# Kernel tuning notes

Measured on AMD Instinct MI355X. Metric: run time of the kernel, lower is better.

## Reference

```python
import jax, jax.numpy as jnp
import numpy as np

N, IN_DIM, OUT_DIM = 8192, 128, 64
ALPHA = 0.2  # LeakyReLU negative slope
NEG_INF = -1e12


def setup_inputs() -> dict:
    key = jax.random.key(0)
    k1, k2, k3, k4 = jax.random.split(key, 4)
    x = jax.random.normal(k1, (N, IN_DIM), dtype=jnp.float32)
    adj = jax.random.randint(k2, (N, N), 0, 2, dtype=jnp.int32)
    W = jax.random.normal(k3, (IN_DIM, OUT_DIM), dtype=jnp.float32) * 0.1
    a = jax.random.normal(k4, (2 * OUT_DIM, 1), dtype=jnp.float32) * 0.1
    return {"x": x, "adj": adj, "W": W, "a": a}


def reference(x, adj, W, a):
    Wh = x @ W                                   # [N, out_dim]
    Wh1 = Wh @ a[:OUT_DIM, :]                    # [N, 1] source scores
    Wh2 = Wh @ a[OUT_DIM:, :]                    # [N, 1] target scores
    e = Wh1 + Wh2.T                              # [N, N] additive attention
    e = jnp.where(e > 0, e, ALPHA * e)           # LeakyReLU
    scores = jnp.where(adj > 0, e, NEG_INF)      # mask non-edges
    attention = jax.nn.softmax(scores, axis=1)   # row-wise softmax
    h_prime = attention @ Wh                     # [N, out_dim]
    return jax.nn.elu(h_prime)
```

## Files before the change

kernel.cpp:

```cpp
#include <hip/hip_runtime.h>


#define N 8192
#define IN_DIM 128
#define OUT_DIM 64
#define ALPHA 0.2f
#define LOG2E 1.44269504088896f
#define JC 4
#define LDP 264

typedef _Float16 half8 __attribute__((ext_vector_type(8)));
typedef _Float16 h2 __attribute__((ext_vector_type(2)));
typedef float f32x4 __attribute__((ext_vector_type(4)));

static __device__ __forceinline__ h2 bc_h2(unsigned u) {
  return __builtin_bit_cast(h2, u);
}

__global__ __launch_bounds__(64) void wh_kernel(
    const float* __restrict__ x, const float* __restrict__ W,
    const float* __restrict__ a, _Float16* __restrict__ Wh_t,
    float* __restrict__ s1L, float* __restrict__ s2L) {
  __shared__ float xs[IN_DIM];
  const int i = blockIdx.x;
  const int t = threadIdx.x;

  xs[t]      = x[(size_t)i * IN_DIM + t];
  xs[t + 64] = x[(size_t)i * IN_DIM + 64 + t];
  __syncthreads();

  float wh = 0.f;
#pragma unroll
  for (int d = 0; d < IN_DIM; ++d) wh = fmaf(xs[d], W[d * OUT_DIM + t], wh);

  Wh_t[(size_t)t * N + i] = (_Float16)wh;

  float p1 = wh * a[t];
  float p2 = wh * a[64 + t];
#pragma unroll
  for (int off = 32; off; off >>= 1) {
    p1 += __shfl_down(p1, off);
    p2 += __shfl_down(p2, off);
  }
  if (t == 0) {
    s1L[i] = p1 * LOG2E;
    s2L[i] = p2 * LOG2E;
  }
}

__global__ __launch_bounds__(256) void max_kernel(
    const float* __restrict__ s1L, const float* __restrict__ s2L,
    float* __restrict__ mm) {
  __shared__ float red[8];
  const int t = threadIdx.x;
  float m1 = -1e30f, m2 = -1e30f;
  for (int idx = t; idx < N; idx += 256) {
    m1 = fmaxf(m1, s1L[idx]);
    m2 = fmaxf(m2, s2L[idx]);
  }
#pragma unroll
  for (int off = 32; off; off >>= 1) {
    m1 = fmaxf(m1, __shfl_down(m1, off));
    m2 = fmaxf(m2, __shfl_down(m2, off));
  }
  if ((t & 63) == 0) {
    red[t >> 6] = m1;
    red[4 + (t >> 6)] = m2;
  }
  __syncthreads();
  if (t == 0) {
    m1 = fmaxf(fmaxf(red[0], red[1]), fmaxf(red[2], red[3]));
    m2 = fmaxf(fmaxf(red[4], red[5]), fmaxf(red[6], red[7]));
    float e = m1 + m2;
    mm[0] = m1;
    mm[1] = fmaxf(e, ALPHA * e);
  }
}

__global__ __launch_bounds__(256) void ftab_kernel(
    const float* __restrict__ s1L, const float* __restrict__ s2L,
    const float* __restrict__ mm, unsigned int* __restrict__ Fi,
    _Float16* __restrict__ TTh) {
  const int j = blockIdx.x * 256 + threadIdx.x;
  const float m1 = mm[0], ML = mm[1];

  const float v1 = s1L[j] - m1;
  h2 f;
  f[0] = (_Float16)exp2f(v1);
  f[1] = (_Float16)exp2f(0.2f * v1);
  Fi[j] = __builtin_bit_cast(unsigned int, f);

  TTh[(j >> 2) * 8 + (j & 3)]     = (_Float16)exp2f(s2L[j] - (ML - m1));
  TTh[(j >> 2) * 8 + 4 + (j & 3)] =
      (_Float16)exp2f(0.2f * s2L[j] - (ML - 0.2f * m1));
}

__global__ __launch_bounds__(256) void bpack_kernel(
    const _Float16* __restrict__ Wh_t, _Float16* __restrict__ Bpack) {
  const int kt = blockIdx.x;
  const int t = threadIdx.x;
  const int fg = t >> 6;
  const int lane = t & 63;
  const int q = (t >> 4) & 3;
  const int r16 = t & 15;
  const half8 v =
      *(const half8*)(Wh_t + (size_t)(fg * 16 + r16) * N + kt * 32 + q * 8);
  *(half8*)(Bpack + ((size_t)(kt * 4 + fg) * 64 + lane) * 8) = v;
}

__global__ __launch_bounds__(256, 2) void attn_kernel(
    const int* __restrict__ adj, const _Float16* __restrict__ Bpack,
    const unsigned int* __restrict__ Fi, const uint4* __restrict__ TT,
    float* __restrict__ accp, float* __restrict__ lp) {
  __shared__ __align__(16) _Float16 Ps[4 * 16 * LDP];

  const int t = threadIdx.x;
  const int w = t >> 6;
  const int lane = t & 63;
  const int q = lane >> 4;
  const int r16 = lane & 15;
  const int i0 = blockIdx.x * 64 + w * 16;
  const int c = blockIdx.y;
  const int jb = c * (N / JC);

  _Float16* Pw = Ps + w * 16 * LDP;
  const _Float16* ldA = Pw + r16 * LDP + q * 8;

  half8 bones;
#pragma unroll
  for (int e = 0; e < 8; ++e)
    bones[e] = (r16 == 0) ? (_Float16)1.0f : (_Float16)0.0f;

  const unsigned fi_all = Fi[i0 + r16];
  const int* apb = adj + (size_t)i0 * N + jb + lane * 4;
  const uint4* ttb = TT + (jb >> 2) + lane;

  f32x4 acc[5] = {{0.f, 0.f, 0.f, 0.f}, {0.f, 0.f, 0.f, 0.f},
                  {0.f, 0.f, 0.f, 0.f}, {0.f, 0.f, 0.f, 0.f},
                  {0.f, 0.f, 0.f, 0.f}};

  for (int jt = 0; jt < (N / JC) / 256; ++jt) {
    const uint4 tt = ttb[jt * 64];

#pragma unroll
    for (int b = 0; b < 4; ++b) {
      int4 av[4];
#pragma unroll
      for (int rr = 0; rr < 4; ++rr)
        av[rr] = *(const int4*)(apb + (size_t)(b * 4 + rr) * N + jt * 256);
#pragma unroll
      for (int rr = 0; rr < 4; ++rr) {
        const int row = b * 4 + rr;
        const unsigned u = __shfl(fi_all, row);
        const h2 f1 = bc_h2((u & 0xFFFFu) * 0x00010001u);
        const h2 f2 = bc_h2((u >> 16) * 0x00010001u);
        const unsigned mlo = (unsigned)(av[rr].x | (av[rr].y << 16)) * 0x3C00u;
        const unsigned mhi = (unsigned)(av[rr].z | (av[rr].w << 16)) * 0x3C00u;
        const h2 plo =
            __builtin_elementwise_max(f1 * bc_h2(tt.x), f2 * bc_h2(tt.z)) *
            bc_h2(mlo);
        const h2 phi =
            __builtin_elementwise_max(f1 * bc_h2(tt.y), f2 * bc_h2(tt.w)) *
            bc_h2(mhi);
        uint2 pw;
        pw.x = __builtin_bit_cast(unsigned, plo);
        pw.y = __builtin_bit_cast(unsigned, phi);
        *(uint2*)(Pw + row * LDP + lane * 4) = pw;
      }
    }

    const int ktb = c * 64 + jt * 8;
#pragma unroll
    for (int ks = 0; ks < 8; ++ks) {
      const half8 aF = *(const half8*)(ldA + ks * 32);
      const _Float16* bp = Bpack + ((size_t)((ktb + ks) * 4) * 64 + lane) * 8;
#pragma unroll
      for (int fg = 0; fg < 4; ++fg) {
        const half8 bf = *(const half8*)(bp + (size_t)fg * 512);
        acc[fg] =
            __builtin_amdgcn_mfma_f32_16x16x32_f16(aF, bf, acc[fg], 0, 0, 0);
      }
      acc[4] =
          __builtin_amdgcn_mfma_f32_16x16x32_f16(aF, bones, acc[4], 0, 0, 0);
    }
  }

#pragma unroll
  for (int fg = 0; fg < 4; ++fg) {
#pragma unroll
    for (int r = 0; r < 4; ++r) {
      accp[((size_t)c * N + i0 + q * 4 + r) * OUT_DIM + fg * 16 + r16] =
          acc[fg][r];
    }
  }
  if (r16 == 0) {
#pragma unroll
    for (int r = 0; r < 4; ++r) lp[(size_t)c * N + i0 + q * 4 + r] = acc[4][r];
  }
}

__global__ __launch_bounds__(256) void reduce_kernel(
    const float* __restrict__ accp, const float* __restrict__ lp,
    float* __restrict__ out) {
  const int tid = blockIdx.x * 256 + threadIdx.x;
  const int i = tid >> 6;
  float s = 0.f, l = 0.f;
#pragma unroll
  for (int c = 0; c < JC; ++c) s += accp[(size_t)c * N * OUT_DIM + tid];
#pragma unroll
  for (int c = 0; c < JC; ++c) l += lp[(size_t)c * N + i];
  float v = s / l;
  out[tid] = v > 0.f ? v : expm1f(v);
}

extern "C" void kernel_launch(void* const* d_in, const int* in_sizes, int n_in,
                              void* d_out, int out_size, void* d_ws,
                              size_t ws_size, hipStream_t stream) {
  const float* x = (const float*)d_in[0];
  const int* adj = (const int*)d_in[1];
  const float* W = (const float*)d_in[2];
  const float* a = (const float*)d_in[3];
  float* out = (float*)d_out;

  char* ws = (char*)d_ws;
  _Float16* Wh_t = (_Float16*)ws;
  float* s1L = (float*)(ws + (1u << 20));
  float* s2L = (float*)(ws + (1u << 20) + (64u << 10));
  float* mm = (float*)(ws + (1u << 20) + (128u << 10));
  unsigned* Fi = (unsigned*)(ws + (1u << 20) + (192u << 10));
  _Float16* TTh = (_Float16*)(ws + (1u << 20) + (256u << 10));
  _Float16* Bpack = (_Float16*)(ws + (2u << 20));
  float* accp = (float*)(ws + (4u << 20));
  float* lp = (float*)(ws + (20u << 20));

  wh_kernel<<<N, 64, 0, stream>>>(x, W, a, Wh_t, s1L, s2L);
  max_kernel<<<1, 256, 0, stream>>>(s1L, s2L, mm);
  ftab_kernel<<<N / 256, 256, 0, stream>>>(s1L, s2L, mm, Fi, TTh);
  bpack_kernel<<<N / 32, 256, 0, stream>>>(Wh_t, Bpack);
  attn_kernel<<<dim3(N / 64, JC), 256, 0, stream>>>(
      adj, Bpack, Fi, (const uint4*)TTh, accp, lp);
  reduce_kernel<<<N * OUT_DIM / 256, 256, 0, stream>>>(accp, lp, out);
}
```

Measured before the change: 442.3 us.

## Share attention tile across waves and keep Wh operands in registers

The attention kernel is reorganized so each block covers 128 rows by 512 columns. The four waves jointly build one 16-row probability tile in shared memory, and each wave multiplies it against its own 16-feature slice of Wh, held in registers for the whole block. Adjacency rows for the next 16-row group are prefetched into registers during the MFMA phase, and only one wave computes the row-sum MFMA. This removes the repeated global loads of packed Wh and the per-wave private P tiles. In exchange, the column split grows to 16 chunks, which quadruples partial-sum traffic for the reduce kernel and adds two block barriers per row group.

```diff
diff --git a/kernel.cpp b/kernel.cpp
--- a/kernel.cpp
+++ b/kernel.cpp
@@ -6,8 +6,9 @@
 #define OUT_DIM 64
 #define ALPHA 0.2f
 #define LOG2E 1.44269504088896f
-#define JC 4
-#define LDP 264
+#define JC 16
+#define LDP 520
+#define RG 8
 
 typedef _Float16 half8 __attribute__((ext_vector_type(8)));
 typedef _Float16 h2 __attribute__((ext_vector_type(2)));
@@ -108,94 +109,97 @@
   *(half8*)(Bpack + ((size_t)(kt * 4 + fg) * 64 + lane) * 8) = v;
 }
 
-__global__ __launch_bounds__(256, 2) void attn_kernel(
+__global__ __launch_bounds__(256, 3) void attn_kernel(
     const int* __restrict__ adj, const _Float16* __restrict__ Bpack,
     const unsigned int* __restrict__ Fi, const uint4* __restrict__ TT,
     float* __restrict__ accp, float* __restrict__ lp) {
-  __shared__ __align__(16) _Float16 Ps[4 * 16 * LDP];
+  __shared__ __align__(16) _Float16 Pb[16 * LDP];
 
   const int t = threadIdx.x;
   const int w = t >> 6;
   const int lane = t & 63;
   const int q = lane >> 4;
   const int r16 = lane & 15;
-  const int i0 = blockIdx.x * 64 + w * 16;
+  const int half_ = lane >> 5;
+  const int l32 = lane & 31;
+  const int ib0 = blockIdx.x * 128;
   const int c = blockIdx.y;
-  const int jb = c * (N / JC);
-
-  _Float16* Pw = Ps + w * 16 * LDP;
-  const _Float16* ldA = Pw + r16 * LDP + q * 8;
+  const int jb = c * 512;
+  const int jw = jb + w * 128;
+
+  half8 bw[16];
+#pragma unroll
+  for (int ks = 0; ks < 16; ++ks)
+    bw[ks] = *(const half8*)(Bpack +
+                             ((size_t)((c * 16 + ks) * 4 + w) * 64 + lane) * 8);
 
   half8 bones;
 #pragma unroll
   for (int e = 0; e < 8; ++e)
     bones[e] = (r16 == 0) ? (_Float16)1.0f : (_Float16)0.0f;
 
-  const unsigned fi_all = Fi[i0 + r16];
-  const int* apb = adj + (size_t)i0 * N + jb + lane * 4;
-  const uint4* ttb = TT + (jb >> 2) + lane;
-
-  f32x4 acc[5] = {{0.f, 0.f, 0.f, 0.f}, {0.f, 0.f, 0.f, 0.f},
-                  {0.f, 0.f, 0.f, 0.f}, {0.f, 0.f, 0.f, 0.f},
-                  {0.f, 0.f, 0.f, 0.f}};
-
-  for (int jt = 0; jt < (N / JC) / 256; ++jt) {
-    const uint4 tt = ttb[jt * 64];
-
-#pragma unroll
-    for (int b = 0; b < 4; ++b) {
-      int4 av[4];
-#pragma unroll
-      for (int rr = 0; rr < 4; ++rr)
-        av[rr] = *(const int4*)(apb + (size_t)(b * 4 + rr) * N + jt * 256);
-#pragma unroll
-      for (int rr = 0; rr < 4; ++rr) {
-        const int row = b * 4 + rr;
-        const unsigned u = __shfl(fi_all, row);
-        const h2 f1 = bc_h2((u & 0xFFFFu) * 0x00010001u);
-        const h2 f2 = bc_h2((u >> 16) * 0x00010001u);
-        const unsigned mlo = (unsigned)(av[rr].x | (av[rr].y << 16)) * 0x3C00u;
-        const unsigned mhi = (unsigned)(av[rr].z | (av[rr].w << 16)) * 0x3C00u;
-        const h2 plo =
-            __builtin_elementwise_max(f1 * bc_h2(tt.x), f2 * bc_h2(tt.z)) *
-            bc_h2(mlo);
-        const h2 phi =
-            __builtin_elementwise_max(f1 * bc_h2(tt.y), f2 * bc_h2(tt.w)) *
-            bc_h2(mhi);
-        uint2 pw;
-        pw.x = __builtin_bit_cast(unsigned, plo);
-        pw.y = __builtin_bit_cast(unsigned, phi);
-        *(uint2*)(Pw + row * LDP + lane * 4) = pw;
-      }
-    }
-
-    const int ktb = c * 64 + jt * 8;
-#pragma unroll
-    for (int ks = 0; ks < 8; ++ks) {
-      const half8 aF = *(const half8*)(ldA + ks * 32);
-      const _Float16* bp = Bpack + ((size_t)((ktb + ks) * 4) * 64 + lane) * 8;
-#pragma unroll
-      for (int fg = 0; fg < 4; ++fg) {
-        const half8 bf = *(const half8*)(bp + (size_t)fg * 512);
-        acc[fg] =
-            __builtin_amdgcn_mfma_f32_16x16x32_f16(aF, bf, acc[fg], 0, 0, 0);
-      }
-      acc[4] =
-          __builtin_amdgcn_mfma_f32_16x16x32_f16(aF, bones, acc[4], 0, 0, 0);
-    }
-  }
-
-#pragma unroll
-  for (int fg = 0; fg < 4; ++fg) {
+  const uint4 tt = TT[(jw >> 2) + l32];
+  const h2 t1lo = bc_h2(tt.x), t1hi = bc_h2(tt.y);
+  const h2 t2lo = bc_h2(tt.z), t2hi = bc_h2(tt.w);
+
+  const int* ap = adj + (size_t)(ib0 + half_) * N + jw + l32 * 4;
+  int4 av[8];
+#pragma unroll
+  for (int it = 0; it < 8; ++it)
+    av[it] = *(const int4*)(ap + (size_t)(2 * it) * N);
+  unsigned fi = Fi[ib0 + r16];
+
+  for (int rg = 0; rg < RG; ++rg) {
+    const int i0 = ib0 + rg * 16;
+
+    __syncthreads();
+
+#pragma unroll
+    for (int it = 0; it < 8; ++it) {
+      const unsigned u = __shfl(fi, 2 * it + half_);
+      const h2 f1 = bc_h2((u & 0xFFFFu) * 0x00010001u);
+      const h2 f2 = bc_h2((u >> 16) * 0x00010001u);
+      const unsigned mlo = (unsigned)(av[it].x | (av[it].y << 16)) * 0x3C00u;
+      const unsigned mhi = (unsigned)(av[it].z | (av[it].w << 16)) * 0x3C00u;
+      const h2 plo =
+          __builtin_elementwise_max(f1 * t1lo, f2 * t2lo) * bc_h2(mlo);
+      const h2 phi =
+          __builtin_elementwise_max(f1 * t1hi, f2 * t2hi) * bc_h2(mhi);
+      uint2 pw;
+      pw.x = __builtin_bit_cast(unsigned, plo);
+      pw.y = __builtin_bit_cast(unsigned, phi);
+      *(uint2*)(Pb + (2 * it + half_) * LDP + w * 128 + l32 * 4) = pw;
+    }
+
+    __syncthreads();
+
+    const int rgn = (rg + 1) & (RG - 1);
+#pragma unroll
+    for (int it = 0; it < 8; ++it)
+      av[it] = *(const int4*)(ap + (size_t)(rgn * 16 + 2 * it) * N);
+    fi = Fi[ib0 + rgn * 16 + r16];
+
+    f32x4 acc = {0.f, 0.f, 0.f, 0.f};
+    f32x4 lacc = {0.f, 0.f, 0.f, 0.f};
+#pragma unroll
+    for (int ks = 0; ks < 16; ++ks) {
+      const half8 aF = *(const half8*)(Pb + r16 * LDP + ks * 32 + q * 8);
+      acc = __builtin_amdgcn_mfma_f32_16x16x32_f16(aF, bw[ks], acc, 0, 0, 0);
+      if (w == 3)
+        lacc =
+            __builtin_amdgcn_mfma_f32_16x16x32_f16(aF, bones, lacc, 0, 0, 0);
+    }
+
 #pragma unroll
     for (int r = 0; r < 4; ++r) {
-      accp[((size_t)c * N + i0 + q * 4 + r) * OUT_DIM + fg * 16 + r16] =
-          acc[fg][r];
-    }
-  }
-  if (r16 == 0) {
-#pragma unroll
-    for (int r = 0; r < 4; ++r) lp[(size_t)c * N + i0 + q * 4 + r] = acc[4][r];
+      accp[((size_t)c * N + i0 + q * 4 + r) * OUT_DIM + w * 16 + r16] =
+          acc[r];
+    }
+    if (w == 3 && r16 == 0) {
+#pragma unroll
+      for (int r = 0; r < 4; ++r)
+        lp[(size_t)c * N + i0 + q * 4 + r] = lacc[r];
+    }
   }
 }
 
@@ -231,13 +235,13 @@
   _Float16* TTh = (_Float16*)(ws + (1u << 20) + (256u << 10));
   _Float16* Bpack = (_Float16*)(ws + (2u << 20));
   float* accp = (float*)(ws + (4u << 20));
-  float* lp = (float*)(ws + (20u << 20));
+  float* lp = (float*)(ws + (40u << 20));
 
   wh_kernel<<<N, 64, 0, stream>>>(x, W, a, Wh_t, s1L, s2L);
   max_kernel<<<1, 256, 0, stream>>>(s1L, s2L, mm);
   ftab_kernel<<<N / 256, 256, 0, stream>>>(s1L, s2L, mm, Fi, TTh);
   bpack_kernel<<<N / 32, 256, 0, stream>>>(Wh_t, Bpack);
-  attn_kernel<<<dim3(N / 64, JC), 256, 0, stream>>>(
+  attn_kernel<<<dim3(N / 128, JC), 256, 0, stream>>>(
       adj, Bpack, Fi, (const uint4*)TTh, accp, lp);
   reduce_kernel<<<N * OUT_DIM / 256, 256, 0, stream>>>(accp, lp, out);
 }
```

Measured after the change: 422.3 us. -4.5%, faster.
